# Optimization experiments

Measured on AMD Instinct MI355X. Metric: run time of the kernel, lower is better.

The kernel has to match this reference:

```python
import jax, jax.numpy as jnp
from jax import lax
import numpy as np


def setup_inputs() -> dict:
    key = jax.random.key(0)
    B, N, K_ORDERS = 8, 16384, 4
    k1, k2 = jax.random.split(key)
    coord = jax.random.normal(k1, (B * N, 3), dtype=jnp.float32)
    serialized_code = jax.random.randint(k2, (K_ORDERS, B * N), 0, 1 << 30)
    return {
        "coord": coord,
        "serialized_code": serialized_code,
        "batch_size": 8,
        "num_group": 1024,
        "group_size": 32,
    }


def _fps(pts, G):
    """Farthest point sampling on pts [N,3]; starts at index 0 (pointops convention)."""
    N = pts.shape[0]

    def step(carry, _):
        dist, last = carry
        d = jnp.sum((pts - pts[last]) ** 2, axis=-1)  # [N]
        dist = jnp.minimum(dist, d)
        nxt = jnp.argmax(dist).astype(jnp.int32)
        return (dist, nxt), nxt

    init = (jnp.full((N,), jnp.inf, pts.dtype), jnp.int32(0))
    _, rest = lax.scan(step, init, None, length=G - 1)
    return jnp.concatenate([jnp.zeros((1,), jnp.int32), rest])  # [G]


def reference(coord, serialized_code, batch_size, num_group, group_size):
    B, G, S = batch_size, num_group, group_size
    N = coord.shape[0] // B
    pts = coord.reshape(B, N, 3)

    # --- FPS per cloud (offset-batched in the original) ---
    loc_idx = jax.vmap(lambda p: _fps(p, G))(pts)  # [B, G] local indices
    s_idx = (loc_idx + (jnp.arange(B, dtype=jnp.int32) * N)[:, None]).reshape(-1)  # [B*G] global
    s_xyz = coord[s_idx]  # [B*G, 3]

    # --- KNN per cloud: S nearest points to each sampled center ---
    centers = s_xyz.reshape(B, G, 3)

    def knn_one(p, c):  # p [N,3], c [G,3]
        # squared distances via gemm to avoid [G,N,3] intermediate
        d2 = (jnp.sum(c * c, -1)[:, None] + jnp.sum(p * p, -1)[None, :]
              - 2.0 * c @ p.T)  # [G, N]
        _, idx = lax.top_k(-d2, S)  # ascending distance, self first
        return idx

    nloc = jax.vmap(knn_one)(pts, centers)  # [B, G, S]
    s_n_idx = (nloc + (jnp.arange(B) * N)[:, None, None]).reshape(B * G, S)

    # relative coords, drop the self point (column 0)
    s_n = coord[s_n_idx] - s_xyz[:, None, :]  # [B*G, S, 3]
    s_n = s_n[:, 1:, :]  # [B*G, S-1, 3]

    # --- serialization order over sampled points + inverse permutation ---
    code_sel = serialized_code[:, s_idx]  # [K, B*G]
    s_order = jnp.argsort(code_sel, axis=1)  # [K, B*G]
    M = s_order.shape[1]
    src = jnp.broadcast_to(jnp.arange(M, dtype=s_order.dtype), s_order.shape)
    rows = jnp.arange(s_order.shape[0])[:, None]
    s_inverse = jnp.zeros_like(s_order).at[rows, s_order].set(src)

    return s_idx, s_n, s_xyz, s_order, s_inverse
```

## Files before the change

kernel.cpp:

```cpp
#include <hip/hip_runtime.h>
#include <hip/hip_bf16.h>
#include <stdint.h>

#define BB 8
#define NN 16384
#define GG 1024
#define SS 32
#define BN (BB*NN)

#define OFF_SIDX 0
#define OFF_SN   8192
#define OFF_SXYZ 770048
#define OFF_ORD  794624
#define OFF_INV  827392

#define WS_SIDX 0
#define WS_KNN  32768

typedef float v2f __attribute__((ext_vector_type(2)));

static __device__ __forceinline__ v2f vmin2(v2f a, v2f b) {
    v2f r; r.x = fminf(a.x, b.x); r.y = fminf(a.y, b.y); return r;
}
static __device__ __forceinline__ v2f vmax2(v2f a, v2f b) {
    v2f r; r.x = fmaxf(a.x, b.x); r.y = fmaxf(a.y, b.y); return r;
}

template<int CTRL, int RM, int BM>
static __device__ __forceinline__ unsigned dpp_umax(unsigned v) {
    unsigned o = (unsigned)__builtin_amdgcn_update_dpp((int)v, (int)v, CTRL, RM, BM, false);
    return o > v ? o : v;
}

template<int CTRL, int RM, int BM>
static __device__ __forceinline__ uint64_t dpp_umin64(uint64_t v) {
    unsigned lo = (unsigned)v, hi = (unsigned)(v >> 32);
    unsigned olo = (unsigned)__builtin_amdgcn_update_dpp((int)lo, (int)lo, CTRL, RM, BM, false);
    unsigned ohi = (unsigned)__builtin_amdgcn_update_dpp((int)hi, (int)hi, CTRL, RM, BM, false);
    uint64_t o = ((uint64_t)ohi << 32) | olo;
    return o < v ? o : v;
}

static __device__ __forceinline__ uint64_t wave_umin64(uint64_t v) {
    v = dpp_umin64<0x111, 0xf, 0xf>(v);
    v = dpp_umin64<0x112, 0xf, 0xf>(v);
    v = dpp_umin64<0x114, 0xf, 0xf>(v);
    v = dpp_umin64<0x118, 0xf, 0xf>(v);
    v = dpp_umin64<0x142, 0xa, 0xf>(v);
    v = dpp_umin64<0x143, 0xc, 0xf>(v);
    return v;
}

static __device__ __forceinline__ uint64_t rdlane64(uint64_t v, int sl) {
    unsigned lo = (unsigned)__builtin_amdgcn_readlane((int)(unsigned)v, sl);
    unsigned hi = (unsigned)__builtin_amdgcn_readlane((int)(unsigned)(v >> 32), sl);
    return ((uint64_t)hi << 32) | lo;
}

static __device__ __forceinline__ unsigned mono(float f) {
    unsigned u = __float_as_uint(f);
    return u ^ (unsigned)((((int)u) >> 31) | (int)0x80000000u);
}

__global__ __launch_bounds__(1024)
__attribute__((amdgpu_waves_per_eu(4, 4)))
void fps_kernel(const float* __restrict__ coord,
                int* __restrict__ ws_sidx,
                float* __restrict__ out) {
#pragma clang fp contract(off)
    const int b = blockIdx.x;
    const int t = threadIdx.x;
    const int base = b * NN;
    const int wave = t >> 6, lane = t & 63;

    const float q0x = coord[3*base], q0y = coord[3*base+1], q0z = coord[3*base+2];

    const float* my = coord + 3*(base + t*16);

    v2f dist[8];
#pragma unroll
    for (int j = 0; j < 8; j++) {
        v2f px = (v2f){my[6*j  ], my[6*j+3]};
        v2f py = (v2f){my[6*j+1], my[6*j+4]};
        v2f pz = (v2f){my[6*j+2], my[6*j+5]};
        v2f dx = px - (v2f){q0x,q0x};
        v2f dy = py - (v2f){q0y,q0y};
        v2f dz = pz - (v2f){q0z,q0z};
        dist[j] = (dx*dx + dy*dy) + dz*dz;
    }

    __shared__ unsigned wv[16];
    __shared__ unsigned win[2];

    if (t == 0) {
        ws_sidx[b*GG] = base;
        out[OFF_SIDX + b*GG] = (float)base;
        win[0] = 0xffffffffu; win[1] = 0xffffffffu;
    }
    __syncthreads();

    for (int g = 1; g < GG; g++) {
        const int s = g & 1;
        v2f m01 = vmax2(dist[0], dist[1]);
        v2f m23 = vmax2(dist[2], dist[3]);
        v2f m45 = vmax2(dist[4], dist[5]);
        v2f m67 = vmax2(dist[6], dist[7]);
        v2f m07 = vmax2(vmax2(m01, m23), vmax2(m45, m67));
        float bvf = fmaxf(m07.x, m07.y);
        unsigned lb = __float_as_uint(bvf);
        unsigned r = lb;
        r = dpp_umax<0x111, 0xf, 0xf>(r);
        r = dpp_umax<0x112, 0xf, 0xf>(r);
        r = dpp_umax<0x114, 0xf, 0xf>(r);
        r = dpp_umax<0x118, 0xf, 0xf>(r);
        r = dpp_umax<0x142, 0xa, 0xf>(r);
        r = dpp_umax<0x143, 0xc, 0xf>(r);
        unsigned wmax = (unsigned)__builtin_amdgcn_readlane((int)r, 63);
        if (lane == 0) wv[wave] = wmax;
        __syncthreads();
        if (t == 0) win[1 - s] = 0xffffffffu;
        unsigned x = wv[lane & 15];
        x = dpp_umax<0x111, 0xf, 0xf>(x);
        x = dpp_umax<0x112, 0xf, 0xf>(x);
        x = dpp_umax<0x114, 0xf, 0xf>(x);
        x = dpp_umax<0x118, 0xf, 0xf>(x);
        unsigned bmax = (unsigned)__builtin_amdgcn_readlane((int)x, 15);
        if (lb == bmax) {
            int e = 15;
#pragma unroll
            for (int jj = 15; jj >= 0; jj--) {
                float v = (jj & 1) ? dist[jj >> 1].y : dist[jj >> 1].x;
                if (__float_as_uint(v) == bmax) e = jj;
            }
            atomicMin(&win[s], (unsigned)(t*16 + e));
        }
        __syncthreads();
        unsigned pw = win[s];
        int sp = __builtin_amdgcn_readfirstlane((int)pw);
        if (t == 0) {
            ws_sidx[b*GG + g] = base + sp;
            out[OFF_SIDX + b*GG + g] = (float)(base + sp);
        }
        float qx = coord[3*(base+sp)];
        float qy = coord[3*(base+sp)+1];
        float qz = coord[3*(base+sp)+2];
        v2f qvx = (v2f){qx,qx}, qvy = (v2f){qy,qy}, qvz = (v2f){qz,qz};
#pragma unroll
        for (int j = 0; j < 8; j++) {
            v2f px = (v2f){my[6*j  ], my[6*j+3]};
            v2f py = (v2f){my[6*j+1], my[6*j+4]};
            v2f pz = (v2f){my[6*j+2], my[6*j+5]};
            v2f dx = px - qvx, dy = py - qvy, dz = pz - qvz;
            v2f d  = (dx*dx + dy*dy) + dz*dz;
            dist[j] = vmin2(dist[j], d);
        }
    }
}

__global__ __launch_bounds__(64) void knn_kernel(const float* __restrict__ coord,
                                                 const int* __restrict__ ws_sidx,
                                                 int* __restrict__ ws_knn) {
#pragma clang fp contract(off)
    const int c = blockIdx.x;
    const int l = threadIdx.x;
    const int b = c >> 10;
    const int base = b * NN;
    const int sg = ws_sidx[c];
    const float cx = coord[3*sg], cy = coord[3*sg+1], cz = coord[3*sg+2];
    const float cc = (cx*cx + cy*cy) + cz*cz;

    uint64_t k1 = ~0ull, k2 = ~0ull;
#pragma unroll 4
    for (int j = 0; j < 256; j++) {
        int p = l + (j << 6);
        float x = coord[3*(base+p)], y = coord[3*(base+p)+1], z = coord[3*(base+p)+2];
        float pp  = (x*x + y*y) + z*z;
        float dot = (cx*x + cy*y) + cz*z;
        float d2  = (cc + pp) - 2.0f*dot;
        uint64_t key = (((uint64_t)mono(d2)) << 14) | (unsigned)p;
        if (key < k1)      { k2 = k1; k1 = key; }
        else if (key < k2) { k2 = key; }
    }

    uint64_t m0 = 0, m1 = 0, m2 = 0, m3 = 0;
    uint64_t cur = k1, nxt = k2;
    bool have_nxt = true;
    int res_p = 0;
    for (int k = 0; k < SS; k++) {
        uint64_t wmin = wave_umin64(cur);
        uint64_t bkey = rdlane64(wmin, 63);
        const int bp = (int)(bkey & 16383u);
        const int w  = bp & 63;
        const int e  = bp >> 6;
        if (l == k) res_p = bp;
        bool need_rescan = false;
        if (l == w) {
            uint64_t bit = 1ull << (e & 63);
            int word = e >> 6;
            if      (word == 0) m0 |= bit;
            else if (word == 1) m1 |= bit;
            else if (word == 2) m2 |= bit;
            else                m3 |= bit;
            if (have_nxt) { cur = nxt; have_nxt = false; }
            else need_rescan = true;
        }
        if (__ballot(need_rescan)) {
            uint64_t w0 = rdlane64(m0, w), w1 = rdlane64(m1, w),
                     w2 = rdlane64(m2, w), w3 = rdlane64(m3, w);
            uint64_t best = ~0ull;
#pragma unroll
            for (int m = 0; m < 4; m++) {
                int e2 = l + (m << 6);
                uint64_t mw = (m == 0) ? w0 : ((m == 1) ? w1 : ((m == 2) ? w2 : w3));
                int p2 = w + (e2 << 6);
                float x = coord[3*(base+p2)], y = coord[3*(base+p2)+1], z = coord[3*(base+p2)+2];
                float pp  = (x*x + y*y) + z*z;
                float dot = (cx*x + cy*y) + cz*z;
                float d2  = (cc + pp) - 2.0f*dot;
                uint64_t key = (((uint64_t)mono(d2)) << 14) | (unsigned)p2;
                bool cons = (mw >> l) & 1ull;
                if (!cons && key < best) best = key;
            }
            best = wave_umin64(best);
            uint64_t rk = rdlane64(best, 63);
            if (l == w) cur = rk;
        }
    }
    if (l < SS) ws_knn[c * SS + l] = res_p;
}

__global__ void sxyz_kernel(const float* __restrict__ coord,
                            const int* __restrict__ ws_sidx,
                            float* __restrict__ out) {
    int t = blockIdx.x * blockDim.x + threadIdx.x;
    if (t < 8192*3) {
        int i = t / 3, cmp = t - 3*i;
        out[OFF_SXYZ + t] = coord[3*ws_sidx[i] + cmp];
    }
}

__global__ void sn_kernel(const float* __restrict__ coord,
                          const int* __restrict__ ws_sidx,
                          const int* __restrict__ ws_knn,
                          float* __restrict__ out) {
#pragma clang fp contract(off)
    int t = blockIdx.x * blockDim.x + threadIdx.x;
    if (t < 8192*31*3) {
        int cmp = t % 3; int rem = t / 3;
        int j = rem % 31; int i = rem / 31;
        int b = i >> 10;
        int nb = ws_knn[i*SS + j + 1];
        int gidx = b*NN + nb;
        float v = coord[3*gidx + cmp] - coord[3*ws_sidx[i] + cmp];
        out[OFF_SN + t] = v;
    }
}

__global__ __launch_bounds__(1024) void sort_kernel(const int* __restrict__ ser,
                                                    const int* __restrict__ ws_sidx,
                                                    float* __restrict__ out) {
    __shared__ uint64_t keys[8192];
    const int r = blockIdx.x, t = threadIdx.x;
#pragma unroll
    for (int s = 0; s < 8; s++) {
        int i = t + (s << 10);
        uint32_t code = (uint32_t)ser[r * BN + ws_sidx[i]];
        keys[i] = ((uint64_t)code << 13) | (uint32_t)i;
    }
    __syncthreads();
    for (int k2 = 2; k2 <= 8192; k2 <<= 1) {
        for (int j = k2 >> 1; j > 0; j >>= 1) {
#pragma unroll 2
            for (int s = 0; s < 8; s++) {
                int i = t + (s << 10);
                int ixj = i ^ j;
                if (ixj > i) {
                    uint64_t a = keys[i], bq = keys[ixj];
                    bool up = ((i & k2) == 0);
                    if ((a > bq) == up) { keys[i] = bq; keys[ixj] = a; }
                }
            }
            __syncthreads();
        }
    }
    for (int s = 0; s < 8; s++) {
        int k = t + (s << 10);
        uint64_t key = keys[k];
        int i = (int)(key & 8191u);
        out[OFF_ORD + r*8192 + k] = (float)i;
        out[OFF_INV + r*8192 + i] = (float)k;
    }
}

extern "C" void kernel_launch(void* const* d_in, const int* in_sizes, int n_in,
                              void* d_out, int out_size, void* d_ws, size_t ws_size,
                              hipStream_t stream) {
    const float* coord = (const float*)d_in[0];
    const int* ser = (const int*)d_in[1];
    float* out = (float*)d_out;
    char* ws = (char*)d_ws;
    int* ws_sidx = (int*)(ws + WS_SIDX);
    int* ws_knn  = (int*)(ws + WS_KNN);

    hipLaunchKernelGGL(fps_kernel,  dim3(BB),   dim3(1024), 0, stream, coord, ws_sidx, out);
    hipLaunchKernelGGL(knn_kernel,  dim3(8192), dim3(64),   0, stream, coord, ws_sidx, ws_knn);
    hipLaunchKernelGGL(sxyz_kernel, dim3(96),   dim3(256),  0, stream, coord, ws_sidx, out);
    hipLaunchKernelGGL(sn_kernel,   dim3(2976), dim3(256),  0, stream, coord, ws_sidx, ws_knn, out);
    hipLaunchKernelGGL(sort_kernel, dim3(4),    dim3(1024), 0, stream, ser, ws_sidx, out);
}
```

Baseline: 1.831 ms.

## Keep bitonic sort keys in registers, exchange partners through shared memory

```diff
diff --git a/kernel.cpp b/kernel.cpp
--- a/kernel.cpp
+++ b/kernel.cpp
@@ -18,6 +18,7 @@
 #define WS_KNN  32768
 
 typedef float v2f __attribute__((ext_vector_type(2)));
+typedef unsigned long long u64x2 __attribute__((ext_vector_type(2)));
 
 static __device__ __forceinline__ v2f vmin2(v2f a, v2f b) {
     v2f r; r.x = fminf(a.x, b.x); r.y = fminf(a.y, b.y); return r;
@@ -259,33 +260,61 @@
 __global__ __launch_bounds__(1024) void sort_kernel(const int* __restrict__ ser,
                                                     const int* __restrict__ ws_sidx,
                                                     float* __restrict__ out) {
-    __shared__ uint64_t keys[8192];
+    __shared__ __align__(16) uint64_t keys[8192];
     const int r = blockIdx.x, t = threadIdx.x;
-#pragma unroll
-    for (int s = 0; s < 8; s++) {
-        int i = t + (s << 10);
+    uint64_t e[8];
+#pragma unroll
+    for (int m = 0; m < 8; m++) {
+        int i = t*8 + m;
         uint32_t code = (uint32_t)ser[r * BN + ws_sidx[i]];
-        keys[i] = ((uint64_t)code << 13) | (uint32_t)i;
-    }
-    __syncthreads();
-    for (int k2 = 2; k2 <= 8192; k2 <<= 1) {
-        for (int j = k2 >> 1; j > 0; j >>= 1) {
-#pragma unroll 2
-            for (int s = 0; s < 8; s++) {
-                int i = t + (s << 10);
-                int ixj = i ^ j;
-                if (ixj > i) {
-                    uint64_t a = keys[i], bq = keys[ixj];
-                    bool up = ((i & k2) == 0);
-                    if ((a > bq) == up) { keys[i] = bq; keys[ixj] = a; }
-                }
+        e[m] = ((uint64_t)code << 13) | (uint32_t)i;
+    }
+#define CE(a, b, up) { uint64_t xa = e[a], xb = e[b]; \
+                       if ((xa > xb) == (up)) { e[a] = xb; e[b] = xa; } }
+    CE(0,1,true) CE(2,3,false) CE(4,5,true) CE(6,7,false)
+    CE(0,2,true) CE(1,3,true) CE(4,6,false) CE(5,7,false)
+    CE(0,1,true) CE(2,3,true) CE(4,5,false) CE(6,7,false)
+    {
+        bool up = ((t & 1) == 0);
+        CE(0,4,up) CE(1,5,up) CE(2,6,up) CE(3,7,up)
+        CE(0,2,up) CE(1,3,up) CE(4,6,up) CE(5,7,up)
+        CE(0,1,up) CE(2,3,up) CE(4,5,up) CE(6,7,up)
+    }
+    u64x2* kp = (u64x2*)keys;
+    for (int k2 = 16; k2 <= 8192; k2 <<= 1) {
+        const bool up = ((t & (k2 >> 3)) == 0);
+        for (int j = k2 >> 1; j >= 8; j >>= 1) {
+#pragma unroll
+            for (int q = 0; q < 4; q++)
+                kp[t*4 + q] = (u64x2){e[2*q], e[2*q+1]};
+            __syncthreads();
+            const int pt = t ^ (j >> 3);
+            uint64_t pb[8];
+#pragma unroll
+            for (int q = 0; q < 4; q++) {
+                u64x2 v = kp[pt*4 + q];
+                pb[2*q] = v.x; pb[2*q+1] = v.y;
+            }
+            const bool lower = ((t & (j >> 3)) == 0);
+            const bool keepmin = (lower == up);
+#pragma unroll
+            for (int m = 0; m < 8; m++) {
+                uint64_t a = e[m], bq = pb[m];
+                uint64_t mn = a < bq ? a : bq;
+                uint64_t mx = a < bq ? bq : a;
+                e[m] = keepmin ? mn : mx;
             }
             __syncthreads();
         }
-    }
-    for (int s = 0; s < 8; s++) {
-        int k = t + (s << 10);
-        uint64_t key = keys[k];
+        CE(0,4,up) CE(1,5,up) CE(2,6,up) CE(3,7,up)
+        CE(0,2,up) CE(1,3,up) CE(4,6,up) CE(5,7,up)
+        CE(0,1,up) CE(2,3,up) CE(4,5,up) CE(6,7,up)
+    }
+#undef CE
+#pragma unroll
+    for (int m = 0; m < 8; m++) {
+        int k = t*8 + m;
+        uint64_t key = e[m];
         int i = (int)(key & 8191u);
         out[OFF_ORD + r*8192 + k] = (float)i;
         out[OFF_INV + r*8192 + i] = (float)k;
```

New measurement: 1.801 ms. Within noise of the previous version (-1.7%).
